# Kernel optimization log

Hardware: AMD Instinct MI355X
Metric: run time of the kernel (lower is better)

Reference implementation:

```python
import jax, jax.numpy as jnp
import numpy as np

N_NODES = 100000
N_EDGES = 1600000
D_IN = 64
D_OUT = 64


def setup_inputs() -> dict:
    key = jax.random.key(0)
    k1, k2, k3, k4 = jax.random.split(key, 4)
    features = jax.random.normal(k1, (N_NODES, D_IN), dtype=jnp.float32)
    src = jax.random.randint(k2, (N_EDGES,), 0, N_NODES, dtype=jnp.int32)
    dst = jax.random.randint(k3, (N_EDGES,), 0, N_NODES, dtype=jnp.int32)
    # nn.Linear(input_dim, output_dim): W is [out, in], bias [out]
    W = jax.random.normal(k4, (D_OUT, D_IN), dtype=jnp.float32) * (1.0 / np.sqrt(D_IN))
    b = jnp.zeros((D_OUT,), dtype=jnp.float32)
    return {"features": features, "src": src, "dst": dst, "W": W, "b": b}


def reference(features, src, dst, W, b):
    # DGL update_all(copy_src('h'), sum('m')): for each node v, h[v] = sum over
    # in-edges (u -> v) of features[u].  Gather at src, segment-sum at dst.
    msgs = features[src]  # [E, D_in]
    agg = jax.ops.segment_sum(msgs, dst, num_segments=features.shape[0])  # [N, D_in]
    # nn.Linear: agg @ W.T + b
    return agg @ W.T + b
```

## Files before the change

### kernel.cpp

```cpp
#include <hip/hip_runtime.h>

#define NN 100000
#define NE 1600000
#define D 64
#define NBKT 782
#define BKT_SHIFT 7
#define BKT_MASK 127
#define SRC_MASK 0x1FFFF
#define EPB 2048
#define NPB ((NE + EPB - 1) / EPB)
#define BINCAP 2560
#define TROWS 16
#define FXSCALE 65536.0f
#define FXINV   (1.0f / 65536.0f)

__device__ __forceinline__ unsigned short f2bf(float f) {
    unsigned u = __float_as_uint(f);
    unsigned r = u + 0x7FFF + ((u >> 16) & 1);
    return (unsigned short)(r >> 16);
}

__global__ __launch_bounds__(256) void transform_kernel(const float* __restrict__ feat,
                                                        const float* __restrict__ W,
                                                        unsigned short* __restrict__ hb,
                                                        int* __restrict__ cursor) {
    if (blockIdx.x < 4) {
        int i = blockIdx.x * 256 + threadIdx.x;
        if (i < NBKT) cursor[i] = i * BINCAP;
    }

    __shared__ float4 rowLds[TROWS][16];
    const int lane = threadIdx.x & 63;
    const int wv   = threadIdx.x >> 6;
    float4 wreg[16];
    const float4* __restrict__ W4 = (const float4*)W;
#pragma unroll
    for (int i = 0; i < 16; ++i) wreg[i] = W4[lane * 16 + i];

    const int nTiles = NN / TROWS;
    for (int tile = blockIdx.x; tile < nTiles; tile += gridDim.x) {
        const int rowBase = tile * TROWS;
        rowLds[threadIdx.x >> 4][threadIdx.x & 15] =
            ((const float4*)(feat + (size_t)(rowBase + (threadIdx.x >> 4)) * D))[threadIdx.x & 15];
        __syncthreads();
        float a0 = 0.f, a1 = 0.f, a2 = 0.f, a3 = 0.f;
#pragma unroll
        for (int k4 = 0; k4 < 16; ++k4) {
            const float4 w  = wreg[k4];
            const float4 r0 = rowLds[wv * 4 + 0][k4];
            const float4 r1 = rowLds[wv * 4 + 1][k4];
            const float4 r2 = rowLds[wv * 4 + 2][k4];
            const float4 r3 = rowLds[wv * 4 + 3][k4];
            a0 += r0.x * w.x + r0.y * w.y + r0.z * w.z + r0.w * w.w;
            a1 += r1.x * w.x + r1.y * w.y + r1.z * w.z + r1.w * w.w;
            a2 += r2.x * w.x + r2.y * w.y + r2.z * w.z + r2.w * w.w;
            a3 += r3.x * w.x + r3.y * w.y + r3.z * w.z + r3.w * w.w;
        }
        const size_t ob = (size_t)(rowBase + wv * 4) * D + lane;
        hb[ob]         = f2bf(a0);
        hb[ob + D]     = f2bf(a1);
        hb[ob + 2 * D] = f2bf(a2);
        hb[ob + 3 * D] = f2bf(a3);
        __syncthreads();
    }
}

__global__ __launch_bounds__(256) void p2_scatter(const int* __restrict__ src,
                                                  const int* __restrict__ dst,
                                                  int* __restrict__ cursor,
                                                  int* __restrict__ binned) {
    __shared__ int hist[NBKT];
    __shared__ int base[NBKT];
    for (int i = threadIdx.x; i < NBKT; i += 256) hist[i] = 0;
    __syncthreads();

    const int lo = blockIdx.x * EPB;
    int pk[8], rk[8], bk[8];
#pragma unroll
    for (int j = 0; j < 8; ++j) {
        const int e = lo + j * 256 + threadIdx.x;
        if (e < NE) {
            const int dv = dst[e];
            const int sv = src[e];
            bk[j] = dv >> BKT_SHIFT;
            pk[j] = sv | ((dv & BKT_MASK) << 17);
        } else {
            bk[j] = -1; pk[j] = 0;
        }
    }
#pragma unroll
    for (int j = 0; j < 8; ++j)
        if (bk[j] >= 0) rk[j] = atomicAdd(&hist[bk[j]], 1);
    __syncthreads();

    for (int i = threadIdx.x; i < NBKT; i += 256) {
        const int c = hist[i];
        base[i] = c ? atomicAdd(&cursor[i], c) : 0;
    }
    __syncthreads();

#pragma unroll
    for (int j = 0; j < 8; ++j)
        if (bk[j] >= 0) binned[base[bk[j]] + rk[j]] = pk[j];
}

__global__ __launch_bounds__(256) void bucket_gather(const uint2* __restrict__ hb2,
                                                     const int* __restrict__ binned,
                                                     const int* __restrict__ cursor,
                                                     const float* __restrict__ bias,
                                                     float4* __restrict__ out4) {
    __shared__ int sAcc[128 * 65];
    const int t = threadIdx.x;
    const int b = blockIdx.x;
    for (int i = t; i < 128 * 65; i += 256) sAcc[i] = 0;
    __syncthreads();

    const int gbase = b * BINCAP;
    int sz = cursor[b] - gbase;
    if (sz > BINCAP) sz = BINCAP;

    const int c4  = t & 15;
    const int grp = t >> 4;

    for (int base = grp * 8; base < sz; base += 128) {
        int   p[8];
        uint2 x[8];
#pragma unroll
        for (int j = 0; j < 8; ++j) {
            int i = base + j;
            p[j] = (i < sz) ? binned[gbase + i] : -1;
        }
#pragma unroll
        for (int j = 0; j < 8; ++j)
            x[j] = (p[j] >= 0) ? hb2[(size_t)(p[j] & SRC_MASK) * 16 + c4]
                               : make_uint2(0u, 0u);
#pragma unroll
        for (int j = 0; j < 8; ++j) {
            if (p[j] >= 0) {
                const int d = (p[j] >> 17) & BKT_MASK;
                int* a = &sAcc[d * 65 + c4 * 4];
                atomicAdd(a + 0, (int)(__uint_as_float(x[j].x << 16)         * FXSCALE));
                atomicAdd(a + 1, (int)(__uint_as_float(x[j].x & 0xFFFF0000u) * FXSCALE));
                atomicAdd(a + 2, (int)(__uint_as_float(x[j].y << 16)         * FXSCALE));
                atomicAdd(a + 3, (int)(__uint_as_float(x[j].y & 0xFFFF0000u) * FXSCALE));
            }
        }
    }
    __syncthreads();

    const float4* __restrict__ bias4 = (const float4*)bias;
    for (int i = t; i < 2048; i += 256) {
        const int r   = i >> 4;
        const int cg  = i & 15;
        const int node = b * 128 + r;
        if (node < NN) {
            const int* a = &sAcc[r * 65 + cg * 4];
            const float4 bv = bias4[cg];
            float4 v;
            v.x = (float)a[0] * FXINV + bv.x;
            v.y = (float)a[1] * FXINV + bv.y;
            v.z = (float)a[2] * FXINV + bv.z;
            v.w = (float)a[3] * FXINV + bv.w;
            out4[(size_t)node * 16 + cg] = v;
        }
    }
}

extern "C" void kernel_launch(void* const* d_in, const int* in_sizes, int n_in,
                              void* d_out, int out_size, void* d_ws, size_t ws_size,
                              hipStream_t stream) {
    const float* feat = (const float*)d_in[0];
    const int*   src  = (const int*)d_in[1];
    const int*   dst  = (const int*)d_in[2];
    const float* W    = (const float*)d_in[3];
    const float* b    = (const float*)d_in[4];
    float* out = (float*)d_out;

    unsigned short* hb = (unsigned short*)d_ws;
    int* binned = (int*)(hb + (size_t)NN * D);
    int* cursor = binned + NBKT * BINCAP;

    transform_kernel<<<2048, 256, 0, stream>>>(feat, W, hb, cursor);
    p2_scatter<<<NPB, 256, 0, stream>>>(src, dst, cursor, binned);
    bucket_gather<<<NBKT, 256, 0, stream>>>((const uint2*)hb, binned, cursor,
                                            b, (float4*)out);
}
```

Measured before the change: 180.7 us.

## Sort bucket edges by destination in LDS and accumulate in registers

The gather kernel now counting-sorts each bucket's edges by local destination in shared memory, using a histogram, a prefix scan and a scatter. Each 16-thread group then sums its nodes' neighbour rows in float registers, replacing the fixed-point LDS atomics. Cursor entries are spread out with a stride of 16 to cut contention on the global atomics. The cost is extra LDS passes and scan barriers, plus load imbalance between groups when node degrees vary.

Result: slower. 199.4 us (+10.4%).

```diff
diff --git a/kernel.cpp b/kernel.cpp
--- a/kernel.cpp
+++ b/kernel.cpp
@@ -10,9 +10,8 @@
 #define EPB 2048
 #define NPB ((NE + EPB - 1) / EPB)
 #define BINCAP 2560
+#define CSTRIDE 16
 #define TROWS 16
-#define FXSCALE 65536.0f
-#define FXINV   (1.0f / 65536.0f)
 
 __device__ __forceinline__ unsigned short f2bf(float f) {
     unsigned u = __float_as_uint(f);
@@ -26,7 +25,7 @@
                                                         int* __restrict__ cursor) {
     if (blockIdx.x < 4) {
         int i = blockIdx.x * 256 + threadIdx.x;
-        if (i < NBKT) cursor[i] = i * BINCAP;
+        if (i < NBKT) cursor[i * CSTRIDE] = i * BINCAP;
     }
 
     __shared__ float4 rowLds[TROWS][16];
@@ -95,7 +94,7 @@
 
     for (int i = threadIdx.x; i < NBKT; i += 256) {
         const int c = hist[i];
-        base[i] = c ? atomicAdd(&cursor[i], c) : 0;
+        base[i] = c ? atomicAdd(&cursor[i * CSTRIDE], c) : 0;
     }
     __syncthreads();
 
@@ -109,60 +108,86 @@
                                                      const int* __restrict__ cursor,
                                                      const float* __restrict__ bias,
                                                      float4* __restrict__ out4) {
-    __shared__ int sAcc[128 * 65];
+    __shared__ int cnt[128];
+    __shared__ int pre[128];
+    __shared__ int sEdge[BINCAP];
     const int t = threadIdx.x;
     const int b = blockIdx.x;
-    for (int i = t; i < 128 * 65; i += 256) sAcc[i] = 0;
+    if (t < 128) cnt[t] = 0;
     __syncthreads();
 
     const int gbase = b * BINCAP;
-    int sz = cursor[b] - gbase;
+    int sz = cursor[b * CSTRIDE] - gbase;
     if (sz > BINCAP) sz = BINCAP;
 
-    const int c4  = t & 15;
-    const int grp = t >> 4;
-
-    for (int base = grp * 8; base < sz; base += 128) {
-        int   p[8];
-        uint2 x[8];
-#pragma unroll
-        for (int j = 0; j < 8; ++j) {
-            int i = base + j;
-            p[j] = (i < sz) ? binned[gbase + i] : -1;
-        }
-#pragma unroll
-        for (int j = 0; j < 8; ++j)
-            x[j] = (p[j] >= 0) ? hb2[(size_t)(p[j] & SRC_MASK) * 16 + c4]
-                               : make_uint2(0u, 0u);
-#pragma unroll
-        for (int j = 0; j < 8; ++j) {
-            if (p[j] >= 0) {
-                const int d = (p[j] >> 17) & BKT_MASK;
-                int* a = &sAcc[d * 65 + c4 * 4];
-                atomicAdd(a + 0, (int)(__uint_as_float(x[j].x << 16)         * FXSCALE));
-                atomicAdd(a + 1, (int)(__uint_as_float(x[j].x & 0xFFFF0000u) * FXSCALE));
-                atomicAdd(a + 2, (int)(__uint_as_float(x[j].y << 16)         * FXSCALE));
-                atomicAdd(a + 3, (int)(__uint_as_float(x[j].y & 0xFFFF0000u) * FXSCALE));
-            }
-        }
-    }
-    __syncthreads();
-
-    const float4* __restrict__ bias4 = (const float4*)bias;
-    for (int i = t; i < 2048; i += 256) {
-        const int r   = i >> 4;
-        const int cg  = i & 15;
-        const int node = b * 128 + r;
-        if (node < NN) {
-            const int* a = &sAcc[r * 65 + cg * 4];
-            const float4 bv = bias4[cg];
-            float4 v;
-            v.x = (float)a[0] * FXINV + bv.x;
-            v.y = (float)a[1] * FXINV + bv.y;
-            v.z = (float)a[2] * FXINV + bv.z;
-            v.w = (float)a[3] * FXINV + bv.w;
-            out4[(size_t)node * 16 + cg] = v;
-        }
+    int pk[10], dd[10], rr[10];
+#pragma unroll
+    for (int it = 0; it < 10; ++it) {
+        const int e = it * 256 + t;
+        if (e < sz) {
+            const int p = binned[gbase + e];
+            dd[it] = (p >> 17) & BKT_MASK;
+            pk[it] = p & SRC_MASK;
+            rr[it] = atomicAdd(&cnt[dd[it]], 1);
+        } else dd[it] = -1;
+    }
+    __syncthreads();
+
+    if (t < 128) pre[t] = cnt[t];
+    __syncthreads();
+    for (int s = 1; s < 128; s <<= 1) {
+        int v = 0;
+        if (t < 128 && t >= s) v = pre[t - s];
+        __syncthreads();
+        if (t < 128) pre[t] += v;
+        __syncthreads();
+    }
+
+#pragma unroll
+    for (int it = 0; it < 10; ++it) {
+        if (dd[it] >= 0)
+            sEdge[pre[dd[it]] - cnt[dd[it]] + rr[it]] = pk[it];
+    }
+    __syncthreads();
+
+    const int q  = t >> 4;
+    const int c4 = t & 15;
+    const float4 bv = ((const float4*)bias)[c4];
+    for (int i = 0; i < 8; ++i) {
+        const int n    = q * 8 + i;
+        const int node = b * 128 + n;
+        if (node >= NN) break;
+        const int end = pre[n];
+        int e = end - cnt[n];
+        float a00=0.f,a01=0.f,a02=0.f,a03=0.f, a10=0.f,a11=0.f,a12=0.f,a13=0.f;
+        float a20=0.f,a21=0.f,a22=0.f,a23=0.f, a30=0.f,a31=0.f,a32=0.f,a33=0.f;
+        for (; e + 4 <= end; e += 4) {
+            const int s0 = sEdge[e+0], s1 = sEdge[e+1], s2 = sEdge[e+2], s3 = sEdge[e+3];
+            const uint2 x0 = hb2[(size_t)s0 * 16 + c4];
+            const uint2 x1 = hb2[(size_t)s1 * 16 + c4];
+            const uint2 x2 = hb2[(size_t)s2 * 16 + c4];
+            const uint2 x3 = hb2[(size_t)s3 * 16 + c4];
+            a00 += __uint_as_float(x0.x << 16); a01 += __uint_as_float(x0.x & 0xFFFF0000u);
+            a02 += __uint_as_float(x0.y << 16); a03 += __uint_as_float(x0.y & 0xFFFF0000u);
+            a10 += __uint_as_float(x1.x << 16); a11 += __uint_as_float(x1.x & 0xFFFF0000u);
+            a12 += __uint_as_float(x1.y << 16); a13 += __uint_as_float(x1.y & 0xFFFF0000u);
+            a20 += __uint_as_float(x2.x << 16); a21 += __uint_as_float(x2.x & 0xFFFF0000u);
+            a22 += __uint_as_float(x2.y << 16); a23 += __uint_as_float(x2.y & 0xFFFF0000u);
+            a30 += __uint_as_float(x3.x << 16); a31 += __uint_as_float(x3.x & 0xFFFF0000u);
+            a32 += __uint_as_float(x3.y << 16); a33 += __uint_as_float(x3.y & 0xFFFF0000u);
+        }
+        for (; e < end; ++e) {
+            const int s0 = sEdge[e];
+            const uint2 x0 = hb2[(size_t)s0 * 16 + c4];
+            a00 += __uint_as_float(x0.x << 16); a01 += __uint_as_float(x0.x & 0xFFFF0000u);
+            a02 += __uint_as_float(x0.y << 16); a03 += __uint_as_float(x0.y & 0xFFFF0000u);
+        }
+        float4 v;
+        v.x = (a00 + a10) + (a20 + a30) + bv.x;
+        v.y = (a01 + a11) + (a21 + a31) + bv.y;
+        v.z = (a02 + a12) + (a22 + a32) + bv.z;
+        v.w = (a03 + a13) + (a23 + a33) + bv.w;
+        out4[(size_t)node * 16 + c4] = v;
     }
 }
 
```
